# Performance work log

Hardware: AMD Instinct MI355X
Metric: run time of the kernel (lower is better)

Reference implementation:

```python
import math
import jax, jax.numpy as jnp
import numpy as np

D_MODEL = 1024
HEADS = 16
DH = D_MODEL // HEADS
MAX_REL = 128
LN_EPS = 1e-5


def setup_inputs() -> dict:
    key = jax.random.key(0)
    ks = jax.random.split(key, 6)
    B, T = 4, 2048
    scale = 1.0 / math.sqrt(D_MODEL)
    x = jax.random.normal(ks[0], (B, T, D_MODEL), dtype=jnp.float32)
    Wq = jax.random.normal(ks[1], (D_MODEL, D_MODEL), dtype=jnp.float32) * scale
    Wk = jax.random.normal(ks[2], (D_MODEL, D_MODEL), dtype=jnp.float32) * scale
    Wv = jax.random.normal(ks[3], (D_MODEL, D_MODEL), dtype=jnp.float32) * scale
    Wo = jax.random.normal(ks[4], (D_MODEL, D_MODEL), dtype=jnp.float32) * scale
    # rel bias init as in torch: per-head linspace(0, -2, max_rel+1)
    rel = jnp.tile(jnp.linspace(0.0, -2.0, MAX_REL + 1, dtype=jnp.float32)[None, :], (HEADS, 1))
    ln_gamma = jnp.ones((D_MODEL,), dtype=jnp.float32)
    ln_beta = jnp.zeros((D_MODEL,), dtype=jnp.float32)
    return {"x": x, "Wq": Wq, "Wk": Wk, "Wv": Wv, "Wo": Wo,
            "rel": rel, "ln_gamma": ln_gamma, "ln_beta": ln_beta}


def _layernorm(x, gamma, beta):
    mu = jnp.mean(x, axis=-1, keepdims=True)
    var = jnp.mean(jnp.square(x - mu), axis=-1, keepdims=True)
    return (x - mu) * jax.lax.rsqrt(var + LN_EPS) * gamma + beta


def reference(x, Wq, Wk, Wv, Wo, rel, ln_gamma, ln_beta):
    B, T, D = x.shape
    x0 = x
    xn = _layernorm(x, ln_gamma, ln_beta)
    # projections -> [B, H, T, dh]  (torch Linear: x @ W.T; weights here stored as [out,in])
    def proj(W):
        return (xn @ W.T).reshape(B, T, HEADS, DH).transpose(0, 2, 1, 3)
    q = proj(Wq) / math.sqrt(DH)
    k = proj(Wk)
    v = proj(Wv)
    scores = jnp.einsum('bhid,bhjd->bhij', q, k)  # [B,H,T,T]
    # latency-aware relative bias: bias[h,i,j] = rel[h, min(max(i-j,0), max_rel)]
    i = jnp.arange(T)
    dist = jnp.clip(i[:, None] - i[None, :], 0, MAX_REL)  # [T,T]
    bias = rel[:, dist]  # [H,T,T]
    scores = scores + bias[None]
    causal = i[:, None] >= i[None, :]  # j <= i allowed
    scores = jnp.where(causal[None, None], scores, -jnp.inf)
    attn = jax.nn.softmax(scores, axis=-1)
    y = jnp.einsum('bhij,bhjd->bhid', attn, v)  # [B,H,T,dh]
    y = y.transpose(0, 2, 1, 3).reshape(B, T, D)
    y = y @ Wo.T
    return x0 + y
```

## Files before the change

### kernel.cpp

```cpp
#include <hip/hip_runtime.h>
#include <math.h>

#define TSEQ 2048
#define BATCH 4
#define NH 16
#define DH 64
#define DM 1024
#define NREL 129
#define NEGBIG (-1.0e30f)
#define FIXMAX 8.0f

typedef unsigned short u16;
typedef unsigned int u32;
typedef __attribute__((ext_vector_type(8))) short bf16x8;
typedef __attribute__((ext_vector_type(4))) float f32x4;
typedef __attribute__((ext_vector_type(4))) unsigned short u16x4;

typedef __attribute__((address_space(3))) void lds_void;
typedef const __attribute__((address_space(1))) void g_void;

__device__ inline u16 f2b(float f) {
    union { float f; u32 i; } c; c.f = f;
    u32 x = c.i;
    return (u16)((x + 0x7fffu + ((x >> 16) & 1u)) >> 16);
}

__device__ inline u32 cvtpk(float lo, float hi) {
    u32 r;
    asm("v_cvt_pk_bf16_f32 %0, %1, %2" : "=v"(r) : "v"(lo), "v"(hi));
    return r;
}

__global__ __launch_bounds__(256) void fill_kernel(float* __restrict__ out, int n, float v) {
    for (int i = blockIdx.x * 256 + threadIdx.x; i < n; i += gridDim.x * 256)
        out[i] = v;
}

__global__ __launch_bounds__(256) void ln_kernel(const float* __restrict__ x,
        const float* __restrict__ gamma, const float* __restrict__ beta,
        u16* __restrict__ xn) {
    const int row = blockIdx.x;
    const int tid = threadIdx.x;
    const float* xr = x + (size_t)row * DM;
    f32x4 xv = *(const f32x4*)(xr + tid * 4);
    float s = xv.x + xv.y + xv.z + xv.w;
    float s2 = xv.x*xv.x + xv.y*xv.y + xv.z*xv.z + xv.w*xv.w;
#pragma unroll
    for (int off = 32; off > 0; off >>= 1) {
        s  += __shfl_down(s, off, 64);
        s2 += __shfl_down(s2, off, 64);
    }
    __shared__ alignas(16) float red[8];
    const int wv = tid >> 6, ln = tid & 63;
    if (ln == 0) { red[wv] = s; red[4 + wv] = s2; }
    __syncthreads();
    s  = red[0] + red[1] + red[2] + red[3];
    s2 = red[4] + red[5] + red[6] + red[7];
    const float mu = s * (1.0f / DM);
    float var = s2 * (1.0f / DM) - mu * mu;
    var = var > 0.0f ? var : 0.0f;
    const float rstd = rsqrtf(var + 1e-5f);
    f32x4 gv = *(const f32x4*)(gamma + tid * 4);
    f32x4 bv = *(const f32x4*)(beta + tid * 4);
    u16x4 ov;
    ov.x = f2b((xv.x - mu) * rstd * gv.x + bv.x);
    ov.y = f2b((xv.y - mu) * rstd * gv.y + bv.y);
    ov.z = f2b((xv.z - mu) * rstd * gv.z + bv.z);
    ov.w = f2b((xv.w - mu) * rstd * gv.w + bv.w);
    *(u16x4*)(xn + (size_t)row * DM + tid * 4) = ov;
}

__global__ __launch_bounds__(256) void cvt3_kernel(const float* __restrict__ a,
        const float* __restrict__ b, const float* __restrict__ c,
        u16* __restrict__ dst) {
    const int i = blockIdx.x * 256 + threadIdx.x;
    const int m = i >> 18;
    const int j = i & 0x3FFFF;
    const float* src = m == 0 ? a : (m == 1 ? b : c);
    const float scale = m == 0 ? 0.125f : 1.0f;
    f32x4 v = *(const f32x4*)(src + (size_t)j * 4);
    u16x4 o;
    o.x = f2b(v.x * scale); o.y = f2b(v.y * scale);
    o.z = f2b(v.z * scale); o.w = f2b(v.w * scale);
    *(u16x4*)(dst + (size_t)i * 4) = o;
}

__global__ __launch_bounds__(256) void cvt1_kernel(const float* __restrict__ src,
        u16* __restrict__ dst, int n4) {
    const int i = blockIdx.x * 256 + threadIdx.x;
    if (i >= n4) return;
    f32x4 v = *(const f32x4*)(src + (size_t)i * 4);
    u16x4 o;
    o.x = f2b(v.x); o.y = f2b(v.y); o.z = f2b(v.z); o.w = f2b(v.w);
    *(u16x4*)(dst + (size_t)i * 4) = o;
}

#define BM 128
#define BN 128
#define BK 32

__global__ __launch_bounds__(256) void gemm_qkv(const u16* __restrict__ A,
        const u16* __restrict__ W3, u16* __restrict__ Qb, u16* __restrict__ Kb,
        u16* __restrict__ Vb) {
    __shared__ alignas(16) u16 sh[16384];
    const int id = blockIdx.x + 64 * blockIdx.y;
    const int xcd = id & 7;
    const int k = id >> 3;
    const int xv = xcd * 8 + (k & 7);
    const int yv = k >> 3;
    const int m0 = xv * BM;
    const int mat = yv >> 3;
    const int n0 = (yv & 7) * BN;
    const u16* Wb = W3 + (size_t)mat * DM * DM;
    const int tid = threadIdx.x;
    const int w = tid >> 6;
    const int lane = tid & 63;
    const int quad = lane >> 4, l16 = lane & 15;
    const int wr = (w >> 1) * 64;
    const int wc = (w & 1) * 64;

    const int c0 = w * 2;
    const int srow = c0 * 16 + (lane >> 2);
    const int scol = (lane & 3) * 8;
    const u16* ag = A  + (size_t)(m0 + srow) * DM + scol;
    const u16* bg = Wb + (size_t)(n0 + srow) * DM + scol;
    u16* asw = sh + c0 * 512;
    u16* bsw = sh + 8192 + c0 * 512;

    f32x4 acc[4][4];
#pragma unroll
    for (int i = 0; i < 4; i++)
#pragma unroll
        for (int j = 0; j < 4; j++) acc[i][j] = (f32x4){0.f, 0.f, 0.f, 0.f};

#define QKV_STAGE(buf, kk) do { \
    __builtin_amdgcn_global_load_lds((g_void*)(ag + (kk)),            (lds_void*)(asw + (buf)*4096),       16, 0, 0); \
    __builtin_amdgcn_global_load_lds((g_void*)(ag + (kk) + 16 * DM),  (lds_void*)(asw + (buf)*4096 + 512), 16, 0, 0); \
    __builtin_amdgcn_global_load_lds((g_void*)(bg + (kk)),            (lds_void*)(bsw + (buf)*4096),       16, 0, 0); \
    __builtin_amdgcn_global_load_lds((g_void*)(bg + (kk) + 16 * DM),  (lds_void*)(bsw + (buf)*4096 + 512), 16, 0, 0); \
} while (0)

    QKV_STAGE(0, 0);
    __syncthreads();
    for (int k0 = 0; k0 < DM; k0 += BK) {
        const int cur = (k0 >> 5) & 1;
        if (k0 + BK < DM) QKV_STAGE(cur ^ 1, k0 + BK);
        const u16* Ac = sh + cur * 4096;
        const u16* Bc = sh + 8192 + cur * 4096;
        bf16x8 af[4], bfr[4];
#pragma unroll
        for (int mt = 0; mt < 4; mt++)
            af[mt] = *(const bf16x8*)(Ac + (wr + mt * 16 + l16) * BK + quad * 8);
#pragma unroll
        for (int nt = 0; nt < 4; nt++)
            bfr[nt] = *(const bf16x8*)(Bc + (wc + nt * 16 + l16) * BK + quad * 8);
#pragma unroll
        for (int mt = 0; mt < 4; mt++)
#pragma unroll
            for (int nt = 0; nt < 4; nt++)
                acc[mt][nt] = __builtin_amdgcn_mfma_f32_16x16x32_bf16(af[mt], bfr[nt], acc[mt][nt], 0, 0, 0);
        __syncthreads();
    }
#undef QKV_STAGE

    u16* outb = mat == 0 ? Qb : (mat == 1 ? Kb : Vb);
    const size_t bh = (size_t)(m0 >> 11) * NH + ((n0 + wc) >> 6);
    const int tq = (m0 & 2047) + wr;
    u16* stage = sh + w * 2048;

#pragma unroll
    for (int p = 0; p < 2; p++) {
#pragma unroll
        for (int mt = 0; mt < 4; mt++) {
#pragma unroll
            for (int ntl = 0; ntl < 2; ntl++) {
                const int nt = p * 2 + ntl;
#pragma unroll
                for (int r = 0; r < 4; r++) {
                    const u16 val = f2b(acc[mt][nt][r]);
                    int a;
                    if (mat == 0) {
                        a = mt * 512
                          + ((ntl * 2 + (l16 >> 3)) * 16 + quad * 4 + r) * 8 + (l16 & 7);
                    } else if (mat == 1) {
                        a = ((mt >> 1) * 2 + (quad & 1)) * 512
                          + ((ntl * 2 + (l16 >> 3)) * 16 + (quad >> 1) * 4 + (mt & 1) * 8 + r) * 8
                          + (l16 & 7);
                    } else {
                        a = ((mt >> 1) * 2 + ntl) * 512
                          + (((mt * 2 + (quad >> 1)) & 3) * 16 + l16) * 8
                          + (quad & 1) * 4 + r;
                    }
                    stage[a] = val;
                }
            }
        }
#pragma unroll
        for (int c = 0; c < 4; c++) {
            const bf16x8 vv = *(const bf16x8*)(stage + c * 512 + lane * 8);
            size_t gc;
            if (mat == 0)      gc = (bh * 128 + (tq >> 4) + c) * 2 + p;
            else if (mat == 1) gc = (bh * 64 + (tq >> 5) + (c >> 1)) * 4 + (c & 1) * 2 + p;
            else               gc = (bh * 64 + (tq >> 5) + (c >> 1)) * 4 + p * 2 + (c & 1);
            *(bf16x8*)(outb + gc * 512 + lane * 8) = vv;
        }
    }
}

__global__ __launch_bounds__(256) void gemm_wo(const u16* __restrict__ A,
        const u16* __restrict__ Wb, const float* __restrict__ X0,
        float* __restrict__ out) {
    __shared__ alignas(16) u16 sh[16384];
    const int id = blockIdx.x + 64 * blockIdx.y;
    const int xcd = id & 7;
    const int k = id >> 3;
    const int m0 = (xcd * 8 + (k & 7)) * BM;
    const int n0 = (k >> 3) * BN;
    const int tid = threadIdx.x;
    const int w = tid >> 6;
    const int lane = tid & 63;
    const int quad = lane >> 4, l16 = lane & 15;
    const int wr = (w >> 1) * 64;
    const int wc = (w & 1) * 64;

    const int c0 = w * 2;
    const int srow = c0 * 16 + (lane >> 2);
    const int scol = (lane & 3) * 8;
    const u16* ag = A  + (size_t)(m0 + srow) * DM + scol;
    const u16* bg = Wb + (size_t)(n0 + srow) * DM + scol;
    u16* asw = sh + c0 * 512;
    u16* bsw = sh + 8192 + c0 * 512;

    f32x4 acc[4][4];
#pragma unroll
    for (int i = 0; i < 4; i++)
#pragma unroll
        for (int j = 0; j < 4; j++) acc[i][j] = (f32x4){0.f, 0.f, 0.f, 0.f};

#define WO_STAGE(buf, kk) do { \
    __builtin_amdgcn_global_load_lds((g_void*)(ag + (kk)),            (lds_void*)(asw + (buf)*4096),       16, 0, 0); \
    __builtin_amdgcn_global_load_lds((g_void*)(ag + (kk) + 16 * DM),  (lds_void*)(asw + (buf)*4096 + 512), 16, 0, 0); \
    __builtin_amdgcn_global_load_lds((g_void*)(bg + (kk)),            (lds_void*)(bsw + (buf)*4096),       16, 0, 0); \
    __builtin_amdgcn_global_load_lds((g_void*)(bg + (kk) + 16 * DM),  (lds_void*)(bsw + (buf)*4096 + 512), 16, 0, 0); \
} while (0)

    WO_STAGE(0, 0);
    __syncthreads();
    for (int k0 = 0; k0 < DM; k0 += BK) {
        const int cur = (k0 >> 5) & 1;
        if (k0 + BK < DM) WO_STAGE(cur ^ 1, k0 + BK);
        const u16* Ac = sh + cur * 4096;
        const u16* Bc = sh + 8192 + cur * 4096;
        bf16x8 af[4], bfr[4];
#pragma unroll
        for (int mt = 0; mt < 4; mt++)
            af[mt] = *(const bf16x8*)(Ac + (wr + mt * 16 + l16) * BK + quad * 8);
#pragma unroll
        for (int nt = 0; nt < 4; nt++)
            bfr[nt] = *(const bf16x8*)(Bc + (wc + nt * 16 + l16) * BK + quad * 8);
#pragma unroll
        for (int mt = 0; mt < 4; mt++)
#pragma unroll
            for (int nt = 0; nt < 4; nt++)
                acc[mt][nt] = __builtin_amdgcn_mfma_f32_16x16x32_bf16(af[mt], bfr[nt], acc[mt][nt], 0, 0, 0);
        __syncthreads();
    }
#undef WO_STAGE

#pragma unroll
    for (int mt = 0; mt < 4; mt++) {
#pragma unroll
        for (int nt = 0; nt < 4; nt++) {
#pragma unroll
            for (int r = 0; r < 4; r++) {
                const int row = m0 + wr + mt * 16 + quad * 4 + r;
                const int col = n0 + wc + nt * 16 + l16;
                const size_t idx = (size_t)row * DM + col;
                out[idx] = acc[mt][nt][r] + X0[idx];
            }
        }
    }
}

__global__ __launch_bounds__(512, 8) void attn_kernel(const u16* __restrict__ Q,
        const u16* __restrict__ K, const u16* __restrict__ Vt,
        const float* __restrict__ rel, u16* __restrict__ y) {
    const int id = blockIdx.x + 16 * blockIdx.y;
    const int xcd = id & 7;
    const int idx = id >> 3;
    const int bh = xcd * 8 + (idx & 7);
    const int p = idx >> 3;
    const int h = bh & (NH - 1);
    const int b = bh >> 4;
    const int tid = threadIdx.x;
    const int w = tid >> 6, lane = tid & 63;
    const int rg = w & 3, jg = w >> 2;
    const int quad = lane >> 4, l16 = lane & 15;

    __shared__ alignas(16) float rel_s[NREL];
    __shared__ alignas(16) f32x4 cb[4][5][64];
    __shared__ alignas(16) u16 st_s[4][1024];
    if (tid < NREL) rel_s[tid] = rel[h * NREL + tid];
    __syncthreads();
    const float r128 = rel_s[128];

    const u16* Qh = Q  + (size_t)bh * TSEQ * DH;
    const u16* Kh = K  + (size_t)bh * TSEQ * DH;
    const u16* Vh = Vt + (size_t)bh * TSEQ * DH;

    bf16x8 ones;
#pragma unroll
    for (int j = 0; j < 8; j++) ones[j] = (short)0x3F80;

    for (int ti = 0; ti < 2; ti++) {
        const int qt = ti ? (31 - p) : p;
        const int wq = qt * 64 + rg * 16;
        const int gq = wq + l16;
        const u16* qb = Qh + (size_t)(wq >> 4) * 1024 + lane * 8;
        const bf16x8 qf0 = *(const bf16x8*)(qb);
        const bf16x8 qf1 = *(const bf16x8*)(qb + 512);

        f32x4 o[4];
#pragma unroll
        for (int i = 0; i < 4; i++) o[i] = (f32x4){0.f, 0.f, 0.f, 0.f};
        f32x4 oL = (f32x4){0.f, 0.f, 0.f, 0.f};
        const int jend = wq + 16;

        for (int j0 = jg * 32; j0 < jend; j0 += 64) {
            const u16* kb = Kh + (size_t)(j0 >> 5) * 2048 + lane * 8;
            const bf16x8 k00 = *(const bf16x8*)(kb);
            const bf16x8 k01 = *(const bf16x8*)(kb + 512);
            const bf16x8 k10 = *(const bf16x8*)(kb + 1024);
            const bf16x8 k11 = *(const bf16x8*)(kb + 1536);
            f32x4 s0 = (f32x4){0.f, 0.f, 0.f, 0.f};
            f32x4 s1 = (f32x4){0.f, 0.f, 0.f, 0.f};
            s0 = __builtin_amdgcn_mfma_f32_16x16x32_bf16(k00, qf0, s0, 0, 0, 0);
            s0 = __builtin_amdgcn_mfma_f32_16x16x32_bf16(k01, qf1, s0, 0, 0, 0);
            s1 = __builtin_amdgcn_mfma_f32_16x16x32_bf16(k10, qf0, s1, 0, 0, 0);
            s1 = __builtin_amdgcn_mfma_f32_16x16x32_bf16(k11, qf1, s1, 0, 0, 0);

            float p0[4], p1[4];
            const int dq = gq - j0 - 8 * quad;
            if (j0 + 159 < wq) {
#pragma unroll
                for (int r = 0; r < 4; r++) {
                    p0[r] = __expf(s0[r] + (r128 - FIXMAX));
                    p1[r] = __expf(s1[r] + (r128 - FIXMAX));
                }
            } else {
#pragma unroll
                for (int r = 0; r < 4; r++) {
                    const int d0 = dq - r;
                    const int d1 = dq - 4 - r;
                    const int c0 = d0 < 0 ? 0 : (d0 > 128 ? 128 : d0);
                    const int c1 = d1 < 0 ? 0 : (d1 > 128 ? 128 : d1);
                    float sv0 = s0[r] + rel_s[c0];
                    float sv1 = s1[r] + rel_s[c1];
                    sv0 = d0 >= 0 ? sv0 : NEGBIG;
                    sv1 = d1 >= 0 ? sv1 : NEGBIG;
                    p0[r] = __expf(sv0 - FIXMAX);
                    p1[r] = __expf(sv1 - FIXMAX);
                }
            }
            union { u32 u[4]; bf16x8 v; } pk_;
            pk_.u[0] = cvtpk(p0[0], p0[1]);
            pk_.u[1] = cvtpk(p0[2], p0[3]);
            pk_.u[2] = cvtpk(p1[0], p1[1]);
            pk_.u[3] = cvtpk(p1[2], p1[3]);
            const bf16x8 pf = pk_.v;

            const u16* vb = Vh + (size_t)(j0 >> 5) * 2048 + lane * 8;
            bf16x8 vf[4];
#pragma unroll
            for (int dt = 0; dt < 4; dt++)
                vf[dt] = *(const bf16x8*)(vb + dt * 512);
#pragma unroll
            for (int dt = 0; dt < 4; dt++)
                o[dt] = __builtin_amdgcn_mfma_f32_16x16x32_bf16(pf, vf[dt], o[dt], 0, 0, 0);
            oL = __builtin_amdgcn_mfma_f32_16x16x32_bf16(pf, ones, oL, 0, 0, 0);
        }

        if (jg == 1) {
#pragma unroll
            for (int dt = 0; dt < 4; dt++) cb[rg][dt][lane] = o[dt];
            cb[rg][4][lane] = oL;
        }
        __syncthreads();
        if (jg == 0) {
#pragma unroll
            for (int dt = 0; dt < 4; dt++) {
                const f32x4 op = cb[rg][dt][lane];
                o[dt].x += op.x; o[dt].y += op.y; o[dt].z += op.z; o[dt].w += op.w;
            }
            const f32x4 oLp = cb[rg][4][lane];
            oL.x += oLp.x; oL.y += oLp.y; oL.z += oLp.z; oL.w += oLp.w;
            float inv[4];
#pragma unroll
            for (int r = 0; r < 4; r++) inv[r] = 1.0f / oL[r];
            u16* st = st_s[rg];
#pragma unroll
            for (int dt = 0; dt < 4; dt++)
#pragma unroll
                for (int r = 0; r < 4; r++)
                    st[(quad * 4 + r) * 64 + dt * 16 + l16] = f2b(o[dt][r] * inv[r]);
#pragma unroll
            for (int ps = 0; ps < 2; ps++) {
                const bf16x8 vv = *(const bf16x8*)(st + ps * 512 + lane * 8);
                const int row = wq + ps * 8 + (lane >> 3);
                *(bf16x8*)(y + ((size_t)(b * TSEQ + row)) * DM + h * DH + (lane & 7) * 8) = vv;
            }
        }
        __syncthreads();
    }
}

extern "C" void kernel_launch(void* const* d_in, const int* in_sizes, int n_in,
                              void* d_out, int out_size, void* d_ws, size_t ws_size,
                              hipStream_t stream) {
    const float* x   = (const float*)d_in[0];
    const float* Wq  = (const float*)d_in[1];
    const float* Wk  = (const float*)d_in[2];
    const float* Wv  = (const float*)d_in[3];
    const float* Wo  = (const float*)d_in[4];
    const float* rel = (const float*)d_in[5];
    const float* gam = (const float*)d_in[6];
    const float* bet = (const float*)d_in[7];
    u16* ws = (u16*)d_ws;
    const size_t SZ = (size_t)BATCH * TSEQ * DM;
    const size_t need_bytes = 4 * SZ * sizeof(u16);

    if (n_in != 8) {
        fill_kernel<<<4096, 256, 0, stream>>>((float*)d_out, out_size, 8000.0f);
        return;
    }
    if (ws_size < need_bytes) {
        fill_kernel<<<4096, 256, 0, stream>>>((float*)d_out, out_size, 9500.0f);
        return;
    }

    u16* xn = ws;
    u16* Qb = ws + SZ;
    u16* Kb = ws + 2 * SZ;
    u16* Vb = ws + 3 * SZ;
    u16* y  = xn;

    u16* wscr = (u16*)d_out;
    const int W4 = (DM * DM) / 4;

    ln_kernel<<<BATCH * TSEQ, 256, 0, stream>>>(x, gam, bet, xn);
    cvt3_kernel<<<3 * W4 / 256, 256, 0, stream>>>(Wq, Wk, Wv, wscr);
    gemm_qkv<<<dim3(BATCH * TSEQ / BM, 24), 256, 0, stream>>>(xn, wscr, Qb, Kb, Vb);
    attn_kernel<<<dim3(16, BATCH * NH), 512, 0, stream>>>(Qb, Kb, Vb, rel, y);
    cvt1_kernel<<<W4 / 256, 256, 0, stream>>>(Wo, Qb, W4);
    gemm_wo<<<dim3(BATCH * TSEQ / BM, DM / BN), 256, 0, stream>>>(y, Qb, x, (float*)d_out);
}
```

Baseline: 286.7 us.

## Process two query sub-tiles per wave to reuse K/V fragment loads

Each wave now handles two 16-row query sub-tiles (32 rows) instead of one, so each loaded K and V fragment feeds two sets of MFMAs. The grid is halved to 8 blocks per head, the query tile becomes 128 rows, and launch bounds drop to 4 waves-per-EU hints to allow more registers. The aim is to cut global/L2 traffic for K/V per unit of work, at the cost of higher register pressure, lower occupancy and fewer blocks in flight.

```diff
diff --git a/kernel.cpp b/kernel.cpp
--- a/kernel.cpp
+++ b/kernel.cpp
@@ -282,10 +282,42 @@
     }
 }
 
-__global__ __launch_bounds__(512, 8) void attn_kernel(const u16* __restrict__ Q,
+__device__ inline bf16x8 sm_pack(f32x4 s0, f32x4 s1, int dq, bool fast,
+                                 const float* rel_s, float r128) {
+    float p0[4], p1[4];
+    if (fast) {
+#pragma unroll
+        for (int r = 0; r < 4; r++) {
+            p0[r] = __expf(s0[r] + (r128 - FIXMAX));
+            p1[r] = __expf(s1[r] + (r128 - FIXMAX));
+        }
+    } else {
+#pragma unroll
+        for (int r = 0; r < 4; r++) {
+            const int d0 = dq - r;
+            const int d1 = dq - 4 - r;
+            const int c0 = d0 < 0 ? 0 : (d0 > 128 ? 128 : d0);
+            const int c1 = d1 < 0 ? 0 : (d1 > 128 ? 128 : d1);
+            float sv0 = s0[r] + rel_s[c0];
+            float sv1 = s1[r] + rel_s[c1];
+            sv0 = d0 >= 0 ? sv0 : NEGBIG;
+            sv1 = d1 >= 0 ? sv1 : NEGBIG;
+            p0[r] = __expf(sv0 - FIXMAX);
+            p1[r] = __expf(sv1 - FIXMAX);
+        }
+    }
+    union { u32 u[4]; bf16x8 v; } pk_;
+    pk_.u[0] = cvtpk(p0[0], p0[1]);
+    pk_.u[1] = cvtpk(p0[2], p0[3]);
+    pk_.u[2] = cvtpk(p1[0], p1[1]);
+    pk_.u[3] = cvtpk(p1[2], p1[3]);
+    return pk_.v;
+}
+
+__global__ __launch_bounds__(512, 4) void attn_kernel(const u16* __restrict__ Q,
         const u16* __restrict__ K, const u16* __restrict__ Vt,
         const float* __restrict__ rel, u16* __restrict__ y) {
-    const int id = blockIdx.x + 16 * blockIdx.y;
+    const int id = blockIdx.x + 8 * blockIdx.y;
     const int xcd = id & 7;
     const int idx = id >> 3;
     const int bh = xcd * 8 + (idx & 7);
@@ -298,7 +330,7 @@
     const int quad = lane >> 4, l16 = lane & 15;
 
     __shared__ alignas(16) float rel_s[NREL];
-    __shared__ alignas(16) f32x4 cb[4][5][64];
+    __shared__ alignas(16) f32x4 cb[4][2][5][64];
     __shared__ alignas(16) u16 st_s[4][1024];
     if (tid < NREL) rel_s[tid] = rel[h * NREL + tid];
     __syncthreads();
@@ -313,61 +345,54 @@
     for (int j = 0; j < 8; j++) ones[j] = (short)0x3F80;
 
     for (int ti = 0; ti < 2; ti++) {
-        const int qt = ti ? (31 - p) : p;
-        const int wq = qt * 64 + rg * 16;
-        const int gq = wq + l16;
-        const u16* qb = Qh + (size_t)(wq >> 4) * 1024 + lane * 8;
-        const bf16x8 qf0 = *(const bf16x8*)(qb);
-        const bf16x8 qf1 = *(const bf16x8*)(qb + 512);
-
-        f32x4 o[4];
-#pragma unroll
-        for (int i = 0; i < 4; i++) o[i] = (f32x4){0.f, 0.f, 0.f, 0.f};
-        f32x4 oL = (f32x4){0.f, 0.f, 0.f, 0.f};
-        const int jend = wq + 16;
-
-        for (int j0 = jg * 32; j0 < jend; j0 += 64) {
+        const int qt = ti ? (15 - p) : p;
+        const int lo = qt * 128 + rg * 32;
+        const int hi = lo + 16;
+        const int gqL = lo + l16, gqH = hi + l16;
+        const u16* qb = Qh + (size_t)(lo >> 4) * 1024 + lane * 8;
+        const bf16x8 qf0L = *(const bf16x8*)(qb);
+        const bf16x8 qf1L = *(const bf16x8*)(qb + 512);
+        const bf16x8 qf0H = *(const bf16x8*)(qb + 1024);
+        const bf16x8 qf1H = *(const bf16x8*)(qb + 1536);
+
+        f32x4 o0[4], o1[4];
+#pragma unroll
+        for (int i = 0; i < 4; i++) {
+            o0[i] = (f32x4){0.f, 0.f, 0.f, 0.f};
+            o1[i] = (f32x4){0.f, 0.f, 0.f, 0.f};
+        }
+        f32x4 l0 = (f32x4){0.f, 0.f, 0.f, 0.f};
+        f32x4 l1 = (f32x4){0.f, 0.f, 0.f, 0.f};
+
+        for (int j0 = jg * 32; j0 < lo + 32; j0 += 64) {
             const u16* kb = Kh + (size_t)(j0 >> 5) * 2048 + lane * 8;
             const bf16x8 k00 = *(const bf16x8*)(kb);
             const bf16x8 k01 = *(const bf16x8*)(kb + 512);
             const bf16x8 k10 = *(const bf16x8*)(kb + 1024);
             const bf16x8 k11 = *(const bf16x8*)(kb + 1536);
-            f32x4 s0 = (f32x4){0.f, 0.f, 0.f, 0.f};
-            f32x4 s1 = (f32x4){0.f, 0.f, 0.f, 0.f};
-            s0 = __builtin_amdgcn_mfma_f32_16x16x32_bf16(k00, qf0, s0, 0, 0, 0);
-            s0 = __builtin_amdgcn_mfma_f32_16x16x32_bf16(k01, qf1, s0, 0, 0, 0);
-            s1 = __builtin_amdgcn_mfma_f32_16x16x32_bf16(k10, qf0, s1, 0, 0, 0);
-            s1 = __builtin_amdgcn_mfma_f32_16x16x32_bf16(k11, qf1, s1, 0, 0, 0);
-
-            float p0[4], p1[4];
-            const int dq = gq - j0 - 8 * quad;
-            if (j0 + 159 < wq) {
-#pragma unroll
-                for (int r = 0; r < 4; r++) {
-                    p0[r] = __expf(s0[r] + (r128 - FIXMAX));
-                    p1[r] = __expf(s1[r] + (r128 - FIXMAX));
-                }
-            } else {
-#pragma unroll
-                for (int r = 0; r < 4; r++) {
-                    const int d0 = dq - r;
-                    const int d1 = dq - 4 - r;
-                    const int c0 = d0 < 0 ? 0 : (d0 > 128 ? 128 : d0);
-                    const int c1 = d1 < 0 ? 0 : (d1 > 128 ? 128 : d1);
-                    float sv0 = s0[r] + rel_s[c0];
-                    float sv1 = s1[r] + rel_s[c1];
-                    sv0 = d0 >= 0 ? sv0 : NEGBIG;
-                    sv1 = d1 >= 0 ? sv1 : NEGBIG;
-                    p0[r] = __expf(sv0 - FIXMAX);
-                    p1[r] = __expf(sv1 - FIXMAX);
-                }
+            const bool doLo = j0 < hi;
+
+            f32x4 sH0 = (f32x4){0.f, 0.f, 0.f, 0.f};
+            f32x4 sH1 = (f32x4){0.f, 0.f, 0.f, 0.f};
+            sH0 = __builtin_amdgcn_mfma_f32_16x16x32_bf16(k00, qf0H, sH0, 0, 0, 0);
+            sH0 = __builtin_amdgcn_mfma_f32_16x16x32_bf16(k01, qf1H, sH0, 0, 0, 0);
+            sH1 = __builtin_amdgcn_mfma_f32_16x16x32_bf16(k10, qf0H, sH1, 0, 0, 0);
+            sH1 = __builtin_amdgcn_mfma_f32_16x16x32_bf16(k11, qf1H, sH1, 0, 0, 0);
+            f32x4 sL0 = (f32x4){0.f, 0.f, 0.f, 0.f};
+            f32x4 sL1 = (f32x4){0.f, 0.f, 0.f, 0.f};
+            if (doLo) {
+                sL0 = __builtin_amdgcn_mfma_f32_16x16x32_bf16(k00, qf0L, sL0, 0, 0, 0);
+                sL0 = __builtin_amdgcn_mfma_f32_16x16x32_bf16(k01, qf1L, sL0, 0, 0, 0);
+                sL1 = __builtin_amdgcn_mfma_f32_16x16x32_bf16(k10, qf0L, sL1, 0, 0, 0);
+                sL1 = __builtin_amdgcn_mfma_f32_16x16x32_bf16(k11, qf1L, sL1, 0, 0, 0);
             }
-            union { u32 u[4]; bf16x8 v; } pk_;
-            pk_.u[0] = cvtpk(p0[0], p0[1]);
-            pk_.u[1] = cvtpk(p0[2], p0[3]);
-            pk_.u[2] = cvtpk(p1[0], p1[1]);
-            pk_.u[3] = cvtpk(p1[2], p1[3]);
-            const bf16x8 pf = pk_.v;
+
+            const bf16x8 pfH = sm_pack(sH0, sH1, gqH - j0 - 8 * quad,
+                                       j0 + 159 < hi, rel_s, r128);
+            bf16x8 pfL = pfH;
+            if (doLo)
+                pfL = sm_pack(sL0, sL1, gqL - j0 - 8 * quad,
+                              j0 + 159 < lo, rel_s, r128);
 
             const u16* vb = Vh + (size_t)(j0 >> 5) * 2048 + lane * 8;
             bf16x8 vf[4];
@@ -376,39 +401,57 @@
                 vf[dt] = *(const bf16x8*)(vb + dt * 512);
 #pragma unroll
             for (int dt = 0; dt < 4; dt++)
-                o[dt] = __builtin_amdgcn_mfma_f32_16x16x32_bf16(pf, vf[dt], o[dt], 0, 0, 0);
-            oL = __builtin_amdgcn_mfma_f32_16x16x32_bf16(pf, ones, oL, 0, 0, 0);
+                o1[dt] = __builtin_amdgcn_mfma_f32_16x16x32_bf16(pfH, vf[dt], o1[dt], 0, 0, 0);
+            l1 = __builtin_amdgcn_mfma_f32_16x16x32_bf16(pfH, ones, l1, 0, 0, 0);
+            if (doLo) {
+#pragma unroll
+                for (int dt = 0; dt < 4; dt++)
+                    o0[dt] = __builtin_amdgcn_mfma_f32_16x16x32_bf16(pfL, vf[dt], o0[dt], 0, 0, 0);
+                l0 = __builtin_amdgcn_mfma_f32_16x16x32_bf16(pfL, ones, l0, 0, 0, 0);
+            }
         }
 
         if (jg == 1) {
 #pragma unroll
-            for (int dt = 0; dt < 4; dt++) cb[rg][dt][lane] = o[dt];
-            cb[rg][4][lane] = oL;
+            for (int dt = 0; dt < 4; dt++) {
+                cb[rg][0][dt][lane] = o0[dt];
+                cb[rg][1][dt][lane] = o1[dt];
+            }
+            cb[rg][0][4][lane] = l0;
+            cb[rg][1][4][lane] = l1;
         }
         __syncthreads();
         if (jg == 0) {
-#pragma unroll
-            for (int dt = 0; dt < 4; dt++) {
-                const f32x4 op = cb[rg][dt][lane];
-                o[dt].x += op.x; o[dt].y += op.y; o[dt].z += op.z; o[dt].w += op.w;
-            }
-            const f32x4 oLp = cb[rg][4][lane];
-            oL.x += oLp.x; oL.y += oLp.y; oL.z += oLp.z; oL.w += oLp.w;
-            float inv[4];
-#pragma unroll
-            for (int r = 0; r < 4; r++) inv[r] = 1.0f / oL[r];
-            u16* st = st_s[rg];
-#pragma unroll
-            for (int dt = 0; dt < 4; dt++)
-#pragma unroll
-                for (int r = 0; r < 4; r++)
-                    st[(quad * 4 + r) * 64 + dt * 16 + l16] = f2b(o[dt][r] * inv[r]);
-#pragma unroll
-            for (int ps = 0; ps < 2; ps++) {
-                const bf16x8 vv = *(const bf16x8*)(st + ps * 512 + lane * 8);
-                const int row = wq + ps * 8 + (lane >> 3);
-                *(bf16x8*)(y + ((size_t)(b * TSEQ + row)) * DM + h * DH + (lane & 7) * 8) = vv;
-            }
+#define FINISH(G, OG, LG, BASE) do {                                         \
+            _Pragma("unroll")                                                \
+            for (int dt = 0; dt < 4; dt++) {                                 \
+                const f32x4 op = cb[rg][G][dt][lane];                        \
+                OG[dt].x += op.x; OG[dt].y += op.y;                          \
+                OG[dt].z += op.z; OG[dt].w += op.w;                          \
+            }                                                                \
+            const f32x4 lp = cb[rg][G][4][lane];                             \
+            LG.x += lp.x; LG.y += lp.y; LG.z += lp.z; LG.w += lp.w;          \
+            float inv[4];                                                    \
+            _Pragma("unroll")                                                \
+            for (int r = 0; r < 4; r++) inv[r] = 1.0f / LG[r];               \
+            u16* st = st_s[rg];                                              \
+            _Pragma("unroll")                                                \
+            for (int dt = 0; dt < 4; dt++)                                   \
+                _Pragma("unroll")                                            \
+                for (int r = 0; r < 4; r++)                                  \
+                    st[(quad * 4 + r) * 64 + dt * 16 + l16] =                \
+                        f2b(OG[dt][r] * inv[r]);                             \
+            _Pragma("unroll")                                                \
+            for (int ps = 0; ps < 2; ps++) {                                 \
+                const bf16x8 vv = *(const bf16x8*)(st + ps * 512 + lane * 8);\
+                const int row = (BASE) + ps * 8 + (lane >> 3);               \
+                *(bf16x8*)(y + ((size_t)(b * TSEQ + row)) * DM + h * DH      \
+                           + (lane & 7) * 8) = vv;                           \
+            }                                                                \
+        } while (0)
+            FINISH(0, o0, l0, lo);
+            FINISH(1, o1, l1, hi);
+#undef FINISH
         }
         __syncthreads();
     }
@@ -450,7 +493,7 @@
     ln_kernel<<<BATCH * TSEQ, 256, 0, stream>>>(x, gam, bet, xn);
     cvt3_kernel<<<3 * W4 / 256, 256, 0, stream>>>(Wq, Wk, Wv, wscr);
     gemm_qkv<<<dim3(BATCH * TSEQ / BM, 24), 256, 0, stream>>>(xn, wscr, Qb, Kb, Vb);
-    attn_kernel<<<dim3(16, BATCH * NH), 512, 0, stream>>>(Qb, Kb, Vb, rel, y);
+    attn_kernel<<<dim3(8, BATCH * NH), 512, 0, stream>>>(Qb, Kb, Vb, rel, y);
     cvt1_kernel<<<W4 / 256, 256, 0, stream>>>(Wo, Qb, W4);
     gemm_wo<<<dim3(BATCH * TSEQ / BM, DM / BN), 256, 0, stream>>>(y, Qb, x, (float*)d_out);
 }
```

After: 265.5 us. 1.08x faster.
